# Kernel tuning notes

Measured on AMD Instinct MI355X. Metric: run time of the kernel, lower is better.

Reference implementation:

```python
import jax, jax.numpy as jnp
import numpy as np

J = 3
J_H = 5
C_IN = 128
C_OUT = 128
N0, N1, N2 = 1024, 3072, 2048
DENSITY = 0.01
W_SCALE = 0.02  # keeps P^(2^(J_h-1)) @ x @ W magnitudes reasonable in fp32


def _sym_sparse(key, n, density):
    kv, km = jax.random.split(key)
    mask = jax.random.uniform(km, (n, n)) < density
    a = jnp.where(mask, jax.random.normal(kv, (n, n)), 0.0)
    return jnp.triu(a) + jnp.triu(a, 1).T  # symmetric sparse 'Laplacian'


def _sparse(kv, km, shape, density):
    mask = jax.random.uniform(km, shape) < density
    return jnp.where(mask, jax.random.normal(kv, shape), 0.0)


def setup_inputs() -> dict:
    key = jax.random.key(0)
    ks = jax.random.split(key, 24)
    z0 = jax.random.normal(ks[0], (N0, C_IN), jnp.float32)
    z1 = jax.random.normal(ks[1], (N1, C_IN), jnp.float32)
    z2 = jax.random.normal(ks[2], (N2, C_IN), jnp.float32)
    L0 = _sym_sparse(ks[3], N0, 0.02)
    L1_d = _sym_sparse(ks[4], N1, DENSITY)
    L1_u = _sym_sparse(ks[5], N1, DENSITY)
    L2 = _sym_sparse(ks[6], N2, DENSITY)
    B1 = _sparse(ks[7], ks[8], (N0, N1), DENSITY)
    B2 = _sparse(ks[9], ks[10], (N1, N2), DENSITY)
    W_d = jax.random.normal(ks[11], (J, C_IN, C_OUT)) * W_SCALE
    W_u = jax.random.normal(ks[12], (J, C_IN, C_OUT)) * W_SCALE
    W_h = jax.random.normal(ks[13], (C_IN, C_OUT)) * W_SCALE
    W_b1 = jax.random.normal(ks[14], (J, C_IN, C_OUT)) * W_SCALE
    W_b2 = jax.random.normal(ks[15], (J, C_IN, C_OUT)) * W_SCALE
    attn_d_w = jax.random.normal(ks[16], (1, 2 * C_IN)) * W_SCALE
    attn_d_b = jax.random.normal(ks[17], (1,)) * W_SCALE
    attn_u_w = jax.random.normal(ks[18], (1, 2 * C_IN)) * W_SCALE
    attn_u_b = jax.random.normal(ks[19], (1,)) * W_SCALE
    return dict(z0=z0, z1=z1, z2=z2, L0=L0, L1_d=L1_d, L1_u=L1_u, L2=L2,
                B1=B1, B2=B2, W_d=W_d, W_u=W_u, W_h=W_h, W_b1=W_b1, W_b2=W_b2,
                attn_d_w=attn_d_w, attn_d_b=attn_d_b,
                attn_u_w=attn_u_w, attn_u_b=attn_u_b)


def _attention(x, n, w, b, src, dst):
    # gather edge endpoints -> tiny MLP -> sigmoid -> symmetric scatter
    a = jnp.concatenate([x[src], x[dst]], axis=-1)      # [E, 2C]
    s = jax.nn.sigmoid(a @ w.T + b)[:, 0]               # [E]
    return jnp.zeros((n, n), x.dtype).at[src, dst].set(s).at[dst, src].set(s)


def _harmonic(L, x, W_h):
    lmax = jnp.linalg.eigvalsh(L)[-1]
    # torch does lambda_max.item() -> constant w.r.t. grads
    eps = jax.lax.stop_gradient(jnp.where(lmax > 0, 1.0 / lmax, 0.1))
    P = jnp.eye(L.shape[0], dtype=x.dtype) - eps * L
    for _ in range(J_H - 1):
        P = P @ P                                        # P^(2^(J_h-1))
    return P @ x @ W_h


def reference(z0, z1, z2, L0, L1_d, L1_u, L2, B1, B2,
              W_d, W_u, W_h, W_b1, W_b2,
              attn_d_w, attn_d_b, attn_u_w, attn_u_b):
    # nonzero patterns of the Laplacians (constants, computed on host)
    src_d, dst_d = np.nonzero(np.asarray(jax.device_get(L1_d)))
    src_u, dst_u = np.nonzero(np.asarray(jax.device_get(L1_u)))
    L1d_attn = _attention(z1, N1, attn_d_w, attn_d_b,
                          jnp.asarray(src_d), jnp.asarray(dst_d))
    L1u_attn = _attention(z1, N1, attn_u_w, attn_u_b,
                          jnp.asarray(src_u), jnp.asarray(dst_u))
    # sum_j (A @ z) @ W[j] == (A @ z) @ W.sum(0)
    Wd_s, Wu_s = W_d.sum(0), W_u.sum(0)
    Wb1_s, Wb2_s = W_b1.sum(0), W_b2.sum(0)

    z0_out = (L0 @ z0) @ Wd_s + (B1 @ z1) @ Wb1_s + _harmonic(L0, z0, W_h)
    z0_out = jax.nn.relu(z0_out)

    z1_out = ((L1d_attn @ z1) @ Wd_s + (L1u_attn @ z1) @ Wu_s
              + (B1.T @ z0) @ Wb1_s + (B2 @ z2) @ Wb2_s
              + _harmonic(L1_d + L1_u, z1, W_h))
    z1_out = jax.nn.relu(z1_out)

    z2_out = (L2 @ z2) @ Wu_s + (B2.T @ z1) @ Wb2_s + _harmonic(L2, z2, W_h)
    z2_out = jax.nn.relu(z2_out)
    return (z0_out, z1_out, z2_out)
```

## Files before the change

kernel.cpp:

```cpp
#include <hip/hip_runtime.h>
#include <string.h>

constexpr int M_LZ = 48;

constexpr int CAP_L0 = 26240, CAP_L1 = 118016, CAP_L2 = 52480, CAP_B1 = 39360, CAP_B2 = 78720;
constexpr int CB_L0 = 0;
constexpr int CB_L1D = CB_L0 + CAP_L0;
constexpr int CB_L1U = CB_L1D + CAP_L1;
constexpr int CB_L2  = CB_L1U + CAP_L1;
constexpr int CB_B1  = CB_L2 + CAP_L2;
constexpr int CB_B2  = CB_B1 + CAP_B1;
constexpr int CAP_TOT= CB_B2 + CAP_B2;
constexpr int CB_B1T = CAP_TOT;
constexpr int CB_B2T = CB_B1T + CAP_B1;
constexpr int CAP_TOT2 = CB_B2T + CAP_B2;

constexpr int P_L0=0, P_L1D=1025, P_L1U=4098, P_L2=7171, P_B1=9220, P_B2=10245;
constexpr int P_B1T=13320, P_B2T=16393;
constexpr int C_L0=0, C_L1D=1024, C_L1U=4096, C_L2=7168, C_B1=9216, C_B2=10240;
constexpr int C_B1T=13312, C_B2T=16384;

constexpr size_t HBUF  = (size_t)6144*128;

constexpr size_t W_CNT = 0;
constexpr size_t W_PTR = 18432;
constexpr size_t W_CUR = W_PTR + 18444;
constexpr size_t W_CIDX= W_CUR + 5120;
constexpr size_t W_VAL = W_CIDX + CAP_TOT2;
constexpr size_t W_V0  = W_VAL + CAP_TOT2;
constexpr size_t W_PK  = W_V0 + 6144;
constexpr size_t W_TT  = W_PK + (size_t)64*6144*4;
constexpr size_t W_EPS = W_TT + 6144;
constexpr size_t W_UV  = W_EPS + 128;
constexpr size_t W_H   = W_UV + 4*3072;
constexpr size_t W_SCAT= W_H + 15*HBUF;
constexpr size_t S0_OFF= 0;
constexpr size_t S1_OFF= (size_t)1024*384;
constexpr size_t S2_OFF= S1_OFF + (size_t)3072*640;
constexpr size_t SCAT_TOT = S2_OFF + (size_t)2048*384;
constexpr size_t W_WCAT= W_SCAT + SCAT_TOT;
constexpr size_t WC0=0, WC1=(size_t)384*128, WC2=WC1+(size_t)640*128;
constexpr size_t W_SLOT= W_WCAT + (size_t)1408*128;
constexpr size_t W_FLG = W_SLOT + 1048576;
constexpr size_t W_REL = W_FLG + 65536;

__device__ __forceinline__ float wredf(float v){
  #pragma unroll
  for(int o=32;o;o>>=1) v += __shfl_xor(v,o,64);
  return v;
}
__device__ __forceinline__ int wredi(int v){
  #pragma unroll
  for(int o=32;o;o>>=1) v += __shfl_xor(v,o,64);
  return v;
}
__device__ __forceinline__ void red4x2(float4& a0, float4& a1){
  #pragma unroll
  for (int o=16;o<=32;o<<=1){
    a0.x+=__shfl_xor(a0.x,o,64); a0.y+=__shfl_xor(a0.y,o,64);
    a0.z+=__shfl_xor(a0.z,o,64); a0.w+=__shfl_xor(a0.w,o,64);
    a1.x+=__shfl_xor(a1.x,o,64); a1.y+=__shfl_xor(a1.y,o,64);
    a1.z+=__shfl_xor(a1.z,o,64); a1.w+=__shfl_xor(a1.w,o,64);
  }
}
__device__ __forceinline__ float v0hash(int i, float invs){
  unsigned uu=(unsigned)i*2654435761u; uu^=uu>>16; uu*=2246822519u; uu^=uu>>13;
  return (uu&1)?invs:-invs;
}

__device__ __forceinline__ float ldc(const float* p){
  return __hip_atomic_load(p, __ATOMIC_RELAXED, __HIP_MEMORY_SCOPE_AGENT);
}
__device__ __forceinline__ float2 ldc2(const float* p){
  unsigned long long u = __hip_atomic_load((const unsigned long long*)p,
                          __ATOMIC_RELAXED, __HIP_MEMORY_SCOPE_AGENT);
  float2 r; memcpy(&r,&u,8); return r;
}
__device__ __forceinline__ void stc(float* p, float v){
  __hip_atomic_store(p, v, __ATOMIC_RELAXED, __HIP_MEMORY_SCOPE_AGENT);
}
__device__ __forceinline__ void stc2(float* p, float2 v){
  unsigned long long u; memcpy(&u,&v,8);
  __hip_atomic_store((unsigned long long*)p, u, __ATOMIC_RELAXED, __HIP_MEMORY_SCOPE_AGENT);
}
__device__ __forceinline__ int ldci(const int* p){
  return __hip_atomic_load(p, __ATOMIC_RELAXED, __HIP_MEMORY_SCOPE_AGENT);
}
__device__ __forceinline__ void stci(int* p, int v){
  __hip_atomic_store(p, v, __ATOMIC_RELAXED, __HIP_MEMORY_SCOPE_AGENT);
}

__device__ __forceinline__ void barg(float* ws, int* leafs, int b, int lbase, int Ng,
                                     bool chk, int lidx, int ph){
  const int t = threadIdx.x;
  int* flg = (int*)ws + W_FLG;
  __builtin_amdgcn_s_waitcnt(0);
  __syncthreads();
  if (t==0) stci(flg + (size_t)b*32, ph+1);
  if (chk){
    for (int s=t; s<Ng; s+=256){
      const int* f = flg + (size_t)(lbase+s)*32;
      while (ldci(f) < ph+1) __builtin_amdgcn_s_sleep(1);
    }
    __syncthreads();
    if (t==0){
      #pragma unroll
      for (int i=0;i<16;i++) stci(leafs + (size_t)i*32, ph+1);
    }
    __syncthreads();
  } else {
    if (t==0){
      const int* rl = leafs + (size_t)(lidx&15)*32;
      while (ldci(rl) < ph+1) __builtin_amdgcn_s_sleep(1);
    }
    __syncthreads();
  }
}

__device__ __forceinline__ void bar_lz(float* ws, int b, int grp, int lbase, int Lg,
                                       bool chk, int lb, int ph, int j,
                                       float* shr, float* redm,
                                       float& a_o, float& g_o, float& ib_o){
  const int t = threadIdx.x, lane = t&63, wvv = t>>6;
  __builtin_amdgcn_s_waitcnt(0);
  __syncthreads();
  if (t==0){
    float A0=redm[0]+redm[1]+redm[2]+redm[3];
    float G0=redm[4]+redm[5]+redm[6]+redm[7];
    float N0=redm[8]+redm[9]+redm[10]+redm[11];
    float* sl = ws + W_SLOT + ((size_t)j*2048 + b)*8;
    stc2(sl+2, make_float2(A0,G0)); stc(sl+4, N0);
    __builtin_amdgcn_s_waitcnt(0);
    stci((int*)sl, ph+1);
  }
  if (chk){
    float pa=0.f, pg=0.f, pn=0.f;
    for (int s=t; s<Lg; s+=256){
      const float* sl = ws + W_SLOT + ((size_t)j*2048 + lbase+s)*8;
      while (ldci((const int*)sl) < ph+1) __builtin_amdgcn_s_sleep(1);
      float2 ag = ldc2(sl+2); float nn = ldc(sl+4);
      pa+=ag.x; pg+=ag.y; pn+=nn;
    }
    pa=wredf(pa); pg=wredf(pg); pn=wredf(pn);
    if (lane==0){ shr[0*4+wvv]=pa; shr[1*4+wvv]=pg; shr[2*4+wvv]=pn; }
    __syncthreads();
    if (t==0){
      float a=shr[0]+shr[1]+shr[2]+shr[3];
      float g=shr[4]+shr[5]+shr[6]+shr[7];
      float n=shr[8]+shr[9]+shr[10]+shr[11];
      float ib = 1.f/sqrtf(fmaxf(n - a*a - g*g, 1e-20f));
      float* TT = ws + W_TT + (size_t)(grp*64 + j)*32;
      stc2(TT, make_float2(a,g)); stc(TT+2, n);
      #pragma unroll
      for (int i=0;i<16;i++){
        float* lf = ws + W_REL + (size_t)(grp*16+i)*32;
        stc2(lf+2, make_float2(a,g)); stc(lf+4, ib);
      }
      __builtin_amdgcn_s_waitcnt(0);
      #pragma unroll
      for (int i=0;i<16;i++)
        stci((int*)(ws + W_REL) + (size_t)(grp*16+i)*32, ph+1);
      shr[0]=a; shr[1]=g; shr[2]=ib;
    }
    __syncthreads();
  } else {
    if (t==0){
      const float* lf = ws + W_REL + (size_t)(grp*16 + (lb&15))*32;
      while (ldci((const int*)lf) < ph+1) __builtin_amdgcn_s_sleep(1);
      float2 ag = ldc2(lf+2); float ib = ldc(lf+4);
      shr[0]=ag.x; shr[1]=ag.y; shr[2]=ib;
    }
    __syncthreads();
  }
  a_o = shr[0]; g_o = shr[1]; ib_o = shr[2];
}

__global__ void k_wprep(const float* Wd,const float* Wu,const float* Wh,
                        const float* Wb1,const float* Wb2, float* ws){
  int t = blockIdx.x*256 + threadIdx.x;
  if (t >= 16384) return;
  int* wsi = (int*)ws;
  if (t < 5120) stci(wsi + W_CNT + 13312 + t, 0);
  if (t < 5120) stci(wsi + W_CUR + t, 0);
  for (int i=t; i<65536+2048; i+=16384) wsi[W_FLG+i] = 0;
  for (int i=t; i<131072; i+=16384) wsi[W_SLOT + (size_t)i*8] = 0;
  float sd = Wd[t]  + Wd[16384+t]  + Wd[32768+t];
  float su = Wu[t]  + Wu[16384+t]  + Wu[32768+t];
  float s1 = Wb1[t] + Wb1[16384+t] + Wb1[32768+t];
  float s2 = Wb2[t] + Wb2[16384+t] + Wb2[32768+t];
  float wh = Wh[t];
  float* W0 = ws + W_WCAT + WC0;
  float* W1 = ws + W_WCAT + WC1;
  float* W2 = ws + W_WCAT + WC2;
  W0[t]=sd; W0[16384+t]=s1; W0[32768+t]=wh;
  W1[t]=sd; W1[16384+t]=su; W1[32768+t]=s1; W1[49152+t]=s2; W1[65536+t]=wh;
  W2[t]=su; W2[16384+t]=s2; W2[32768+t]=wh;
}

__device__ __forceinline__ void mat_meta(int wid, const float* L0,const float* L1d,const float* L1u,
    const float* L2,const float* B1,const float* B2,
    const float*& M,int& ncol,int& lrow,int& co,int& po,int& cb,int& cap,int& tco){
  if (wid < 1024){ M=L0;  ncol=1024; lrow=wid;        co=C_L0;  po=P_L0;  cb=CB_L0;  cap=CAP_L0; tco=-1; }
  else if (wid < 4096){ M=L1d; ncol=3072; lrow=wid-1024;  co=C_L1D; po=P_L1D; cb=CB_L1D; cap=CAP_L1; tco=-1; }
  else if (wid < 7168){ M=L1u; ncol=3072; lrow=wid-4096;  co=C_L1U; po=P_L1U; cb=CB_L1U; cap=CAP_L1; tco=-1; }
  else if (wid < 9216){ M=L2;  ncol=2048; lrow=wid-7168;  co=C_L2;  po=P_L2;  cb=CB_L2;  cap=CAP_L2; tco=-1; }
  else if (wid < 10240){ M=B1; ncol=3072; lrow=wid-9216;  co=C_B1;  po=P_B1;  cb=CB_B1;  cap=CAP_B1; tco=C_B1T; }
  else { M=B2; ncol=2048; lrow=wid-10240; co=C_B2;  po=P_B2;  cb=CB_B2;  cap=CAP_B2; tco=C_B2T; }
}

__global__ __launch_bounds__(256,8) void k_all(float* ws,
    const float* z0,const float* z1,const float* z2,
    const float* L0,const float* L1d,const float* L1u,
    const float* L2,const float* B1,const float* B2,
    const float* adw,const float* adb,const float* auw,const float* aub,
    float* out){
  const int b = blockIdx.x, t = threadIdx.x;
  const int wv = t>>6, lane = t&63;
  const int sg = lane>>4, chn = lane&15;
  int* wsi=(int*)ws;
  int* ptrm=wsi+W_PTR; int* cnm=wsi+W_CNT;
  int* cidxm=wsi+W_CIDX; float* valm=ws+W_VAL;

  __shared__ float smem[2616];
  float* Sl  = smem;
  float* Wl  = smem + 544;
  float* TTa = smem;
  float* TTb = smem + 64;
  float* redm= smem + 2592;
  float* shr = smem + 2604;

  int* grel = (int*)ws + W_REL + 48*32;
  int* krel = (int*)ws + W_SLOT + 63*2048*8;

  for (int wid = b*4+wv; wid < 13312; wid += 8192){
    const float* M; int ncol,lrow,co,po,cb,cap,tco;
    mat_meta(wid,L0,L1d,L1u,L2,B1,B2,M,ncol,lrow,co,po,cb,cap,tco);
    const float4* row4 = (const float4*)(M + (size_t)lrow*ncol);
    int c = 0;
    for (int j0=0; j0<ncol; j0+=256){
      float4 v = row4[(j0>>2)+lane];
      int n0=v.x!=0.f, n1=v.y!=0.f, n2=v.z!=0.f, n3=v.w!=0.f;
      c += n0+n1+n2+n3;
      if (tco>=0){
        int jb = j0 + lane*4;
        if (n0) atomicAdd(cnm+tco+jb,   1);
        if (n1) atomicAdd(cnm+tco+jb+1, 1);
        if (n2) atomicAdd(cnm+tco+jb+2, 1);
        if (n3) atomicAdd(cnm+tco+jb+3, 1);
      }
    }
    c = wredi(c);
    if (lane==0) stci(cnm+co+lrow, c);
  }
  barg(ws, grel, b, 0, 2048, b==0, b, 0);

  if (b < 8){
    int* lds = (int*)smem;
    const int rows[8]={1024,3072,3072,2048,1024,3072,3072,2048};
    const int cofs[8]={C_L0,C_L1D,C_L1U,C_L2,C_B1,C_B2,C_B1T,C_B2T};
    const int pofs[8]={P_L0,P_L1D,P_L1U,P_L2,P_B1,P_B2,P_B1T,P_B2T};
    int R=rows[b]; const int* c=cnm+cofs[b]; int* p=ptrm+pofs[b];
    int* cc = (b==6)? (wsi+W_CUR) : (b==7)? (wsi+W_CUR+3072) : nullptr;
    int chunk=(R+255)/256;
    int lo=t*chunk, hi=min(R,lo+chunk);
    int s=0;
    for(int i=lo;i<hi;i++) s+=ldci(c+i);
    lds[t]=(float)0, ((int*)lds)[t]=s; __syncthreads();
    if(t==0){ int run=0; for(int i=0;i<256;i++){int x=((int*)lds)[i];((int*)lds)[i]=run;run+=x;} ((int*)lds)[256]=run; }
    __syncthreads();
    int run=((int*)lds)[t];
    for(int i=lo;i<hi;i++){ stci(p+i, run); if(cc) stci(cc+i, run); run+=ldci(c+i); }
    if(t==0) stci(p+R, ((int*)lds)[256]);
  }
  barg(ws, grel, b, 0, 2048, b==0, b, 1);

  for (int wid = b*4+wv; wid < 13312; wid += 8192){
    const float* M; int ncol,lrow,co,po,cb,cap,tco;
    mat_meta(wid,L0,L1d,L1u,L2,B1,B2,M,ncol,lrow,co,po,cb,cap,tco);
    const float4* row4 = (const float4*)(M + (size_t)lrow*ncol);
    int base = ldci(ptrm+po+lrow);
    int run = 0;
    for (int j0=0; j0<ncol; j0+=256){
      float4 v = row4[(j0>>2)+lane];
      int n0=v.x!=0.f, n1=v.y!=0.f, n2=v.z!=0.f, n3=v.w!=0.f;
      int local = n0+n1+n2+n3;
      int incl = local;
      #pragma unroll
      for (int o=1;o<64;o<<=1){
        int tmp = __shfl_up(incl,o,64);
        if (lane>=o) incl += tmp;
      }
      int tot = __shfl(incl,63,64);
      int pos = base + run + incl - local;
      int jb = j0 + lane*4;
      if (n0){ if(pos<cap){stci(cidxm+cb+pos,jb);   stc(valm+cb+pos,v.x);} pos++; }
      if (n1){ if(pos<cap){stci(cidxm+cb+pos,jb+1); stc(valm+cb+pos,v.y);} pos++; }
      if (n2){ if(pos<cap){stci(cidxm+cb+pos,jb+2); stc(valm+cb+pos,v.z);} pos++; }
      if (n3){ if(pos<cap){stci(cidxm+cb+pos,jb+3); stc(valm+cb+pos,v.w);} pos++; }
      run += tot;
    }
  }
  barg(ws, grel, b, 0, 2048, b==0, b, 2);

  const int* ptr=ptrm; const int* cidx=cidxm; const float* val=valm;

  if (b < 768){
    int g, gbase, nb;
    if (b<128){ g=0; gbase=0;   nb=0;    }
    else if (b<512){ g=1; gbase=128; nb=1024; }
    else { g=2; gbase=512; nb=4096; }
    const int lb = b - gbase;
    const int Lg = (g==0)?128:(g==1)?384:256;
    const bool chk = (lb==0);
    const float invsg = (g==0)?0.03125f:(g==1)?0.0180421959f:0.0220970869f;
    const int hw = lane>>5, hl = lane&31;
    const int p  = lb*8 + wv*2 + hw;
    const int gp = nb + p;
    float a=0.f, gmm=0.f, ib=1.f;
    float vp_m1=0.f, vp_m2=0.f, wp_m1=0.f;
    for (int j=0;j<M_LZ;j++){
      float wp=0.f;
      if (j==0){
        #define GZ(PP,CBB) { const int* rp=ptr+PP; int e=rp[p+1]; \
          for (int k=rp[p]+hl;k<e;k+=32){ wp += val[CBB+k]*v0hash(nb+cidx[CBB+k], invsg); } }
        if (g==0){ GZ(P_L0,CB_L0) }
        else if (g==1){ GZ(P_L1D,CB_L1D) GZ(P_L1U,CB_L1U) }
        else { GZ(P_L2,CB_L2) }
        #undef GZ
      } else {
        const float4* pk = (const float4*)(ws + W_PK) + (size_t)(j-1)*6144 + nb;
        #define GP(PP,CBB) { const int* rp=ptr+PP; int e=rp[p+1]; \
          for (int k=rp[p]+hl;k<e;k+=32){ float v=val[CBB+k]; float4 pq=pk[cidx[CBB+k]]; \
            wp += v*((pq.x - a*pq.y - gmm*pq.z)*ib); } }
        if (g==0){ GP(P_L0,CB_L0) }
        else if (g==1){ GP(P_L1D,CB_L1D) GP(P_L1U,CB_L1U) }
        else { GP(P_L2,CB_L2) }
        #undef GP
      }
      #pragma unroll
      for (int o=16;o;o>>=1) wp += __shfl_xor(wp,o,64);
      float rA=0.f, rG=0.f, rN=0.f;
      if (hl==0){
        float vp;
        if (j==0) vp = v0hash(gp, invsg);
        else      vp = (wp_m1 - a*vp_m1 - gmm*vp_m2)*ib;
        float* pkw = ws + W_PK + ((size_t)j*6144 + gp)*4;
        stc2(pkw, make_float2(wp, vp)); stc(pkw+2, vp_m1);
        rA = vp*wp; rG = vp_m1*wp; rN = wp*wp;
        vp_m2 = vp_m1; vp_m1 = vp; wp_m1 = wp;
      }
      rA += __shfl_xor(rA,32,64); rG += __shfl_xor(rG,32,64); rN += __shfl_xor(rN,32,64);
      if (lane==0){ redm[0*4+wv]=rA; redm[1*4+wv]=rG; redm[2*4+wv]=rN; }
      bar_lz(ws, b, g, gbase, Lg, chk, lb, 1+j, j, shr, redm, a, gmm, ib);
    }
    if (chk && t<64){
      int i = t;
      double lo=1e300, hi=-1e300;
      if (i<M_LZ){
        const float* TT = ws + W_TT + (size_t)(g*64 + i)*32;
        float aa=ldc(TT), gg=ldc(TT+1), nn=ldc(TT+2);
        TTa[i]=aa; TTb[i]=sqrtf(fmaxf(nn-aa*aa-gg*gg,1e-20f));
      }
      if (i<M_LZ){
        double r=(i? fabs((double)TTb[i-1]):0.0) + (i<M_LZ-1? fabs((double)TTb[i]):0.0);
        lo=(double)TTa[i]-r; hi=(double)TTa[i]+r;
      }
      #pragma unroll
      for(int o=32;o;o>>=1){ lo=fmin(lo,__shfl_xor(lo,o,64)); hi=fmax(hi,__shfl_xor(hi,o,64)); }
      lo -= 1.0; hi += 1.0;
      for (int round=0; round<4; round++){
        double x = lo + (hi-lo)*(double)(i+1)/65.0;
        double d = 1.0; int cnt2=0;
        for (int k2=0;k2<M_LZ;k2++){
          double bi = k2? (double)TTb[k2-1] : 0.0;
          d = ((double)TTa[k2]-x) - bi*bi/d;
          if (d==0.0) d = -1e-300;
          if (d<0.0) cnt2++;
        }
        double nlo = (cnt2< M_LZ)? x : -1e300;
        double nhi = (cnt2==M_LZ)? x :  1e300;
        #pragma unroll
        for(int o=32;o;o>>=1){ nlo=fmax(nlo,__shfl_xor(nlo,o,64)); nhi=fmin(nhi,__shfl_xor(nhi,o,64)); }
        if (nlo>-1e299) lo=nlo;
        if (nhi< 1e299) hi=nhi;
      }
      double lam = 0.5*(lo+hi);
      if (i==0) stc(ws+W_EPS+(size_t)g*32, (lam>0.0)? (float)(1.0/lam) : 0.1f);
    }
  } else {
    { int widT = (b-768)*4+wv;
      if (widT < 4096){
        int* cur=wsi+W_CUR;
        if (widT < 1024){
          int r=widT;
          int s0=ldci(ptr+P_B1+r); int e=ldci(ptr+P_B1+r+1);
          for(int k=s0+lane;k<e;k+=64){
            int c=ldci(cidx+CB_B1+k); float v=ldc(val+CB_B1+k);
            int pos=atomicAdd(cur+c,1);
            stci(cidxm+CB_B1T+pos,r); stc(valm+CB_B1T+pos,v);
          }
        } else {
          int r=widT-1024;
          int s0=ldci(ptr+P_B2+r); int e=ldci(ptr+P_B2+r+1);
          for(int k=s0+lane;k<e;k+=64){
            int c=ldci(cidx+CB_B2+k); float v=ldc(val+CB_B2+k);
            int pos=atomicAdd(cur+3072+c,1);
            stci(cidxm+CB_B2T+pos,r); stc(valm+CB_B2T+pos,v);
          }
        }
      }
    }
    const int kb = b - 768;
    const int vw = kb*4 + wv;
    if (vw < 3072){
      float2 x  = ((const float2*)(z1+(size_t)vw*128))[lane];
      float2 a0 = ((const float2*)adw)[lane];
      float2 a1 = ((const float2*)adw)[64+lane];
      float2 b0 = ((const float2*)auw)[lane];
      float2 b1 = ((const float2*)auw)[64+lane];
      float ud=x.x*a0.x+x.y*a0.y, vd=x.x*a1.x+x.y*a1.y;
      float uu=x.x*b0.x+x.y*b0.y, vu=x.x*b1.x+x.y*b1.y;
      ud=wredf(ud); vd=wredf(vd); uu=wredf(uu); vu=wredf(vu);
      if(lane==0){ stc(ws+W_UV+vw,ud); stc(ws+W_UV+3072+vw,vd);
                   stc(ws+W_UV+6144+vw,uu); stc(ws+W_UV+9216+vw,vu); }
    }
    int cgP, nbP, lrP; float e0P;
    if (vw < 3072){ cgP=1; nbP=1024; lrP=vw;      e0P=(1.f/28.f); }
    else          { cgP=2; nbP=4096; lrP=vw-3072; e0P=0.0625f;    }
    const bool has2 = (vw >= 4096);
    const int lr2 = vw - 4096;
    for (int k2=1; k2<=16; k2++){
      const float* ybase = ws + W_H + (size_t)(k2>=2? k2-2:0)*HBUF;
      #define KG2(PP,CBB,NBV,ZZV,LRV) { const int* rp=ptr+PP; int e=rp[(LRV)+1]; \
        for (int kk=rp[LRV]+sg; kk<e; kk+=4){ \
          float v=val[CBB+kk]; int q=cidx[CBB+kk]; \
          const float* sr = (k2==1)? (ZZV)+(size_t)q*128 : ybase+(size_t)((NBV)+q)*128; \
          float4 x0=((const float4*)sr)[chn*2], x1=((const float4*)sr)[chn*2+1]; \
          a0.x+=v*x0.x; a0.y+=v*x0.y; a0.z+=v*x0.z; a0.w+=v*x0.w; \
          a1.x+=v*x1.x; a1.y+=v*x1.y; a1.z+=v*x1.z; a1.w+=v*x1.w; \
        } }
      #define KWRITE(CGV,LRV,GRV,E0V) if (lane<16){ \
          float* dst; \
          if (k2<16) dst = ws + W_H + (size_t)(k2-1)*HBUF + (size_t)(GRV)*128; \
          else { \
            if ((CGV)==0)      dst = ws+W_SCAT+S0_OFF+256 + (size_t)(LRV)*384; \
            else if ((CGV)==1) dst = ws+W_SCAT+S1_OFF+512 + (size_t)(LRV)*640; \
            else               dst = ws+W_SCAT+S2_OFF+256 + (size_t)(LRV)*384; \
          } \
          stc2(dst+chn*8,   make_float2((E0V)*a0.x, (E0V)*a0.y)); \
          stc2(dst+chn*8+2, make_float2((E0V)*a0.z, (E0V)*a0.w)); \
          stc2(dst+chn*8+4, make_float2((E0V)*a1.x, (E0V)*a1.y)); \
          stc2(dst+chn*8+6, make_float2((E0V)*a1.z, (E0V)*a1.w)); }
      {
        float4 a0={0.f,0.f,0.f,0.f}, a1={0.f,0.f,0.f,0.f};
        if (cgP==1){ KG2(P_L1D,CB_L1D,1024,z1,lrP) KG2(P_L1U,CB_L1U,1024,z1,lrP) }
        else { KG2(P_L2,CB_L2,4096,z2,lrP) }
        red4x2(a0,a1);
        KWRITE(cgP, lrP, nbP+lrP, e0P)
      }
      if (has2){
        float4 a0={0.f,0.f,0.f,0.f}, a1={0.f,0.f,0.f,0.f};
        KG2(P_L0,CB_L0,0,z0,lr2)
        red4x2(a0,a1);
        KWRITE(0, lr2, lr2, 0.0625f)
      }
      #undef KG2
      #undef KWRITE
      if (k2<16) barg(ws, krel, b, 768, 1280, b==768, kb, k2+3);
    }
    for (int wid2 = kb*4+wv; wid2 < 18432; wid2 += 5120){
      int task,p2;
      if(wid2<1024){task=0;p2=wid2;}
      else if(wid2<2048){task=1;p2=wid2-1024;}
      else if(wid2<5120){task=2;p2=wid2-2048;}
      else if(wid2<8192){task=3;p2=wid2-5120;}
      else if(wid2<11264){task=4;p2=wid2-8192;}
      else if(wid2<13312){task=5;p2=wid2-11264;}
      else if(wid2<16384){task=6;p2=wid2-13312;}
      else {task=7;p2=wid2-16384;}
      const float* in; const int* rp; int cb2; float* outp; int ostride;
      int mode=0; float Vp=0.f, bb=0.f; const float* U=nullptr;
      switch(task){
        case 0: rp=ptr+P_L0;  cb2=CB_L0;  in=z0; outp=ws+W_SCAT+S0_OFF+0;   ostride=384; break;
        case 1: rp=ptr+P_B1;  cb2=CB_B1;  in=z1; outp=ws+W_SCAT+S0_OFF+128; ostride=384; break;
        case 2: rp=ptr+P_L1D; cb2=CB_L1D; in=z1; outp=ws+W_SCAT+S1_OFF+0;   ostride=640;
                mode=1; U=ws+W_UV; Vp=ldc(ws+W_UV+3072+p2); bb=adb[0]; break;
        case 3: rp=ptr+P_L1U; cb2=CB_L1U; in=z1; outp=ws+W_SCAT+S1_OFF+128; ostride=640;
                mode=1; U=ws+W_UV+6144; Vp=ldc(ws+W_UV+9216+p2); bb=aub[0]; break;
        case 4: rp=ptr+P_B2;  cb2=CB_B2;  in=z2; outp=ws+W_SCAT+S1_OFF+384; ostride=640; break;
        case 5: rp=ptr+P_L2;  cb2=CB_L2;  in=z2; outp=ws+W_SCAT+S2_OFF+0;   ostride=384; break;
        case 6: rp=ptr+P_B1T; cb2=CB_B1T; in=z0; outp=ws+W_SCAT+S1_OFF+256; ostride=640; break;
        default:rp=ptr+P_B2T; cb2=CB_B2T; in=z1; outp=ws+W_SCAT+S2_OFF+128; ostride=384; break;
      }
      float4 a0={0.f,0.f,0.f,0.f}, a1={0.f,0.f,0.f,0.f};
      int e=rp[p2+1];
      for (int k=rp[p2]+sg; k<e; k+=4){
        int q = cidx[cb2+k];
        float v;
        if (mode) v = 1.0f/(1.0f+__expf(-(ldc(U+q)+Vp+bb)));
        else v = val[cb2+k];
        const float* sr = in + (size_t)q*128;
        float4 x0 = ((const float4*)sr)[chn*2];
        float4 x1 = ((const float4*)sr)[chn*2+1];
        a0.x+=v*x0.x; a0.y+=v*x0.y; a0.z+=v*x0.z; a0.w+=v*x0.w;
        a1.x+=v*x1.x; a1.y+=v*x1.y; a1.z+=v*x1.z; a1.w+=v*x1.w;
      }
      red4x2(a0, a1);
      if (sg==0){
        float* dst = outp + (size_t)p2*ostride;
        stc2(dst+chn*8,   make_float2(a0.x,a0.y));
        stc2(dst+chn*8+2, make_float2(a0.z,a0.w));
        stc2(dst+chn*8+4, make_float2(a1.x,a1.y));
        stc2(dst+chn*8+6, make_float2(a1.z,a1.w));
      }
    }
  }

  barg(ws, grel, b, 0, 2048, b==1, b, 30);

  { int r = b*4+wv;
    if (r < 6144){
      int cg = (r<1024)?0:(r<4096)?1:2;
      int lr = r - ((cg==0)?0:(cg==1)?1024:4096);
      const float* zz = (cg==0)?z0:(cg==1)?z1:z2;
      float lam0 = (cg==1)?28.f:16.f;
      float eps  = ldc(ws+W_EPS+(size_t)cg*32);
      float rr = eps*lam0;
      float* hc;
      if (cg==0)      hc = ws+W_SCAT+S0_OFF+256 + (size_t)lr*384;
      else if (cg==1) hc = ws+W_SCAT+S1_OFF+512 + (size_t)lr*640;
      else            hc = ws+W_SCAT+S2_OFF+256 + (size_t)lr*384;
      const float BIN[17] = {1.f,16.f,120.f,560.f,1820.f,4368.f,8008.f,11440.f,12870.f,
                             11440.f,8008.f,4368.f,1820.f,560.f,120.f,16.f,1.f};
      float2 acc = ((const float2*)(zz + (size_t)lr*128))[lane];
      float rk = 1.f;
      #pragma unroll
      for (int k2=1;k2<=15;k2++){
        rk *= -rr;
        float2 y = ((const float2*)(ws + W_H + (size_t)(k2-1)*HBUF + (size_t)r*128))[lane];
        float c = BIN[k2]*rk;
        acc.x += c*y.x; acc.y += c*y.y;
      }
      rk *= -rr;
      float2 y16 = ((const float2*)hc)[lane];
      acc.x += rk*y16.x; acc.y += rk*y16.y;
      stc2(hc + (size_t)lane*2, acc);
    }
  }
  barg(ws, grel, b, 0, 2048, b==1, b, 31);

  if (b < 192){
    const float* S; const float* W; float* outp; int K; int blk;
    if (b<32){       S=ws+W_SCAT+S0_OFF; W=ws+W_WCAT+WC0; outp=out;        K=384; blk=b; }
    else if (b<128){ S=ws+W_SCAT+S1_OFF; W=ws+W_WCAT+WC1; outp=out+131072; K=640; blk=b-32; }
    else {           S=ws+W_SCAT+S2_OFF; W=ws+W_WCAT+WC2; outp=out+524288; K=384; blk=b-128; }
    int r0=blk*32;
    int ty=t>>5, tx=t&31;
    float acc[4][4]={};
    for (int k0=0; k0<K; k0+=16){
      {
        int r=t>>3, kq=(t&7)*2;
        const float* src=S+(size_t)(r0+r)*K + k0+kq;
        Sl[r*17+kq]=src[0]; Sl[r*17+kq+1]=src[1];
      }
      {
        int kk=t>>4, cq=(t&15)*8;
        const float* src=W+(size_t)(k0+kk)*128+cq;
        #pragma unroll
        for(int i=0;i<8;i++) Wl[kk*128+cq+i]=src[i];
      }
      __syncthreads();
      #pragma unroll
      for(int k=0;k<16;k++){
        float sv[4], wvv2[4];
        #pragma unroll
        for(int i=0;i<4;i++) sv[i]=Sl[(ty*4+i)*17+k];
        #pragma unroll
        for(int i=0;i<4;i++) wvv2[i]=Wl[k*128+tx+32*i];
        #pragma unroll
        for(int a2=0;a2<4;a2++)
          #pragma unroll
          for(int b2=0;b2<4;b2++) acc[a2][b2]+=sv[a2]*wvv2[b2];
      }
      __syncthreads();
    }
    #pragma unroll
    for(int a2=0;a2<4;a2++)
      #pragma unroll
      for(int b2=0;b2<4;b2++){
        int r=r0+ty*4+a2, col=tx+32*b2;
        outp[(size_t)r*128+col]=fmaxf(acc[a2][b2],0.f);
      }
  }
}

extern "C" void kernel_launch(void* const* d_in, const int* in_sizes, int n_in,
                              void* d_out, int out_size, void* d_ws, size_t ws_size,
                              hipStream_t stream){
  const float* z0 =(const float*)d_in[0];
  const float* z1 =(const float*)d_in[1];
  const float* z2 =(const float*)d_in[2];
  const float* L0 =(const float*)d_in[3];
  const float* L1d=(const float*)d_in[4];
  const float* L1u=(const float*)d_in[5];
  const float* L2 =(const float*)d_in[6];
  const float* B1 =(const float*)d_in[7];
  const float* B2 =(const float*)d_in[8];
  const float* Wd =(const float*)d_in[9];
  const float* Wu =(const float*)d_in[10];
  const float* Wh =(const float*)d_in[11];
  const float* Wb1=(const float*)d_in[12];
  const float* Wb2=(const float*)d_in[13];
  const float* adw=(const float*)d_in[14];
  const float* adb=(const float*)d_in[15];
  const float* auw=(const float*)d_in[16];
  const float* aub=(const float*)d_in[17];
  float* ws=(float*)d_ws;
  float* out=(float*)d_out;

  hipLaunchKernelGGL(k_wprep, dim3(64), dim3(256), 0, stream, Wd,Wu,Wh,Wb1,Wb2,ws);
  hipLaunchKernelGGL(k_all, dim3(2048), dim3(256), 0, stream,
                     ws, z0, z1, z2, L0, L1d, L1u, L2, B1, B2,
                     adw, adb, auw, aub, out);
}
```

Baseline: 804.3 us.

## Defer B1/B2 CSR build to non-Lanczos blocks to overlap with eigen estimation

The dense-to-CSR count, prefix and fill for the incidence matrices B1 and B2 (plus their transposes) leave the initial grid-wide phases and move into the block group that runs in parallel with the Lanczos blocks, after its Chebyshev/power iterations. The early global barriers then cover only the Laplacians, so the Lanczos eigenvalue estimation can start sooner. The cost is four extra group barriers in the second block group and longer work on that side, which could become the new critical path. Helper functions are factored out for count, fill and prefix.

```diff
diff --git a/kernel.cpp b/kernel.cpp
--- a/kernel.cpp
+++ b/kernel.cpp
@@ -208,6 +208,70 @@
   else { M=B2; ncol=2048; lrow=wid-10240; co=C_B2;  po=P_B2;  cb=CB_B2;  cap=CAP_B2; tco=C_B2T; }
 }
 
+__device__ __forceinline__ void do_count(int wid, const float* L0,const float* L1d,const float* L1u,
+    const float* L2,const float* B1,const float* B2, int* cnm, int lane){
+  const float* M; int ncol,lrow,co,po,cb,cap,tco;
+  mat_meta(wid,L0,L1d,L1u,L2,B1,B2,M,ncol,lrow,co,po,cb,cap,tco);
+  const float4* row4 = (const float4*)(M + (size_t)lrow*ncol);
+  int c = 0;
+  for (int j0=0; j0<ncol; j0+=256){
+    float4 v = row4[(j0>>2)+lane];
+    int n0=v.x!=0.f, n1=v.y!=0.f, n2=v.z!=0.f, n3=v.w!=0.f;
+    c += n0+n1+n2+n3;
+    if (tco>=0){
+      int jb = j0 + lane*4;
+      if (n0) atomicAdd(cnm+tco+jb,   1);
+      if (n1) atomicAdd(cnm+tco+jb+1, 1);
+      if (n2) atomicAdd(cnm+tco+jb+2, 1);
+      if (n3) atomicAdd(cnm+tco+jb+3, 1);
+    }
+  }
+  c = wredi(c);
+  if (lane==0) stci(cnm+co+lrow, c);
+}
+
+__device__ __forceinline__ void do_fill(int wid, const float* L0,const float* L1d,const float* L1u,
+    const float* L2,const float* B1,const float* B2,
+    int* ptrm, int* cidxm, float* valm, int lane){
+  const float* M; int ncol,lrow,co,po,cb,cap,tco;
+  mat_meta(wid,L0,L1d,L1u,L2,B1,B2,M,ncol,lrow,co,po,cb,cap,tco);
+  const float4* row4 = (const float4*)(M + (size_t)lrow*ncol);
+  int base = ldci(ptrm+po+lrow);
+  int run = 0;
+  for (int j0=0; j0<ncol; j0+=256){
+    float4 v = row4[(j0>>2)+lane];
+    int n0=v.x!=0.f, n1=v.y!=0.f, n2=v.z!=0.f, n3=v.w!=0.f;
+    int local = n0+n1+n2+n3;
+    int incl = local;
+    #pragma unroll
+    for (int o=1;o<64;o<<=1){
+      int tmp = __shfl_up(incl,o,64);
+      if (lane>=o) incl += tmp;
+    }
+    int tot = __shfl(incl,63,64);
+    int pos = base + run + incl - local;
+    int jb = j0 + lane*4;
+    if (n0){ if(pos<cap){stci(cidxm+cb+pos,jb);   stc(valm+cb+pos,v.x);} pos++; }
+    if (n1){ if(pos<cap){stci(cidxm+cb+pos,jb+1); stc(valm+cb+pos,v.y);} pos++; }
+    if (n2){ if(pos<cap){stci(cidxm+cb+pos,jb+2); stc(valm+cb+pos,v.z);} pos++; }
+    if (n3){ if(pos<cap){stci(cidxm+cb+pos,jb+3); stc(valm+cb+pos,v.w);} pos++; }
+    run += tot;
+  }
+}
+
+__device__ __forceinline__ void do_prefix(int R, const int* c, int* p, int* cc, int* lds, int t){
+  int chunk=(R+255)/256;
+  int lo=t*chunk, hi=min(R,lo+chunk);
+  int s=0;
+  for(int i=lo;i<hi;i++) s+=ldci(c+i);
+  lds[t]=s; __syncthreads();
+  if(t==0){ int run=0; for(int i=0;i<256;i++){int x=lds[i];lds[i]=run;run+=x;} lds[256]=run; }
+  __syncthreads();
+  int run=lds[t];
+  for(int i=lo;i<hi;i++){ stci(p+i, run); if(cc) stci(cc+i, run); run+=ldci(c+i); }
+  if(t==0) stci(p+R, lds[256]);
+}
+
 __global__ __launch_bounds__(256,8) void k_all(float* ws,
     const float* z0,const float* z1,const float* z2,
     const float* L0,const float* L1d,const float* L1u,
@@ -232,74 +296,21 @@
   int* grel = (int*)ws + W_REL + 48*32;
   int* krel = (int*)ws + W_SLOT + 63*2048*8;
 
-  for (int wid = b*4+wv; wid < 13312; wid += 8192){
-    const float* M; int ncol,lrow,co,po,cb,cap,tco;
-    mat_meta(wid,L0,L1d,L1u,L2,B1,B2,M,ncol,lrow,co,po,cb,cap,tco);
-    const float4* row4 = (const float4*)(M + (size_t)lrow*ncol);
-    int c = 0;
-    for (int j0=0; j0<ncol; j0+=256){
-      float4 v = row4[(j0>>2)+lane];
-      int n0=v.x!=0.f, n1=v.y!=0.f, n2=v.z!=0.f, n3=v.w!=0.f;
-      c += n0+n1+n2+n3;
-      if (tco>=0){
-        int jb = j0 + lane*4;
-        if (n0) atomicAdd(cnm+tco+jb,   1);
-        if (n1) atomicAdd(cnm+tco+jb+1, 1);
-        if (n2) atomicAdd(cnm+tco+jb+2, 1);
-        if (n3) atomicAdd(cnm+tco+jb+3, 1);
-      }
-    }
-    c = wredi(c);
-    if (lane==0) stci(cnm+co+lrow, c);
-  }
+  for (int wid = b*4+wv; wid < 9216; wid += 8192)
+    do_count(wid, L0,L1d,L1u,L2,B1,B2, cnm, lane);
   barg(ws, grel, b, 0, 2048, b==0, b, 0);
 
-  if (b < 8){
+  if (b < 4){
     int* lds = (int*)smem;
-    const int rows[8]={1024,3072,3072,2048,1024,3072,3072,2048};
-    const int cofs[8]={C_L0,C_L1D,C_L1U,C_L2,C_B1,C_B2,C_B1T,C_B2T};
-    const int pofs[8]={P_L0,P_L1D,P_L1U,P_L2,P_B1,P_B2,P_B1T,P_B2T};
-    int R=rows[b]; const int* c=cnm+cofs[b]; int* p=ptrm+pofs[b];
-    int* cc = (b==6)? (wsi+W_CUR) : (b==7)? (wsi+W_CUR+3072) : nullptr;
-    int chunk=(R+255)/256;
-    int lo=t*chunk, hi=min(R,lo+chunk);
-    int s=0;
-    for(int i=lo;i<hi;i++) s+=ldci(c+i);
-    lds[t]=(float)0, ((int*)lds)[t]=s; __syncthreads();
-    if(t==0){ int run=0; for(int i=0;i<256;i++){int x=((int*)lds)[i];((int*)lds)[i]=run;run+=x;} ((int*)lds)[256]=run; }
-    __syncthreads();
-    int run=((int*)lds)[t];
-    for(int i=lo;i<hi;i++){ stci(p+i, run); if(cc) stci(cc+i, run); run+=ldci(c+i); }
-    if(t==0) stci(p+R, ((int*)lds)[256]);
+    const int rows[4]={1024,3072,3072,2048};
+    const int cofs[4]={C_L0,C_L1D,C_L1U,C_L2};
+    const int pofs[4]={P_L0,P_L1D,P_L1U,P_L2};
+    do_prefix(rows[b], cnm+cofs[b], ptrm+pofs[b], nullptr, lds, t);
   }
   barg(ws, grel, b, 0, 2048, b==0, b, 1);
 
-  for (int wid = b*4+wv; wid < 13312; wid += 8192){
-    const float* M; int ncol,lrow,co,po,cb,cap,tco;
-    mat_meta(wid,L0,L1d,L1u,L2,B1,B2,M,ncol,lrow,co,po,cb,cap,tco);
-    const float4* row4 = (const float4*)(M + (size_t)lrow*ncol);
-    int base = ldci(ptrm+po+lrow);
-    int run = 0;
-    for (int j0=0; j0<ncol; j0+=256){
-      float4 v = row4[(j0>>2)+lane];
-      int n0=v.x!=0.f, n1=v.y!=0.f, n2=v.z!=0.f, n3=v.w!=0.f;
-      int local = n0+n1+n2+n3;
-      int incl = local;
-      #pragma unroll
-      for (int o=1;o<64;o<<=1){
-        int tmp = __shfl_up(incl,o,64);
-        if (lane>=o) incl += tmp;
-      }
-      int tot = __shfl(incl,63,64);
-      int pos = base + run + incl - local;
-      int jb = j0 + lane*4;
-      if (n0){ if(pos<cap){stci(cidxm+cb+pos,jb);   stc(valm+cb+pos,v.x);} pos++; }
-      if (n1){ if(pos<cap){stci(cidxm+cb+pos,jb+1); stc(valm+cb+pos,v.y);} pos++; }
-      if (n2){ if(pos<cap){stci(cidxm+cb+pos,jb+2); stc(valm+cb+pos,v.z);} pos++; }
-      if (n3){ if(pos<cap){stci(cidxm+cb+pos,jb+3); stc(valm+cb+pos,v.w);} pos++; }
-      run += tot;
-    }
-  }
+  for (int wid = b*4+wv; wid < 9216; wid += 8192)
+    do_fill(wid, L0,L1d,L1u,L2,B1,B2, ptrm, cidxm, valm, lane);
   barg(ws, grel, b, 0, 2048, b==0, b, 2);
 
   const int* ptr=ptrm; const int* cidx=cidxm; const float* val=valm;
@@ -388,28 +399,6 @@
       if (i==0) stc(ws+W_EPS+(size_t)g*32, (lam>0.0)? (float)(1.0/lam) : 0.1f);
     }
   } else {
-    { int widT = (b-768)*4+wv;
-      if (widT < 4096){
-        int* cur=wsi+W_CUR;
-        if (widT < 1024){
-          int r=widT;
-          int s0=ldci(ptr+P_B1+r); int e=ldci(ptr+P_B1+r+1);
-          for(int k=s0+lane;k<e;k+=64){
-            int c=ldci(cidx+CB_B1+k); float v=ldc(val+CB_B1+k);
-            int pos=atomicAdd(cur+c,1);
-            stci(cidxm+CB_B1T+pos,r); stc(valm+CB_B1T+pos,v);
-          }
-        } else {
-          int r=widT-1024;
-          int s0=ldci(ptr+P_B2+r); int e=ldci(ptr+P_B2+r+1);
-          for(int k=s0+lane;k<e;k+=64){
-            int c=ldci(cidx+CB_B2+k); float v=ldc(val+CB_B2+k);
-            int pos=atomicAdd(cur+3072+c,1);
-            stci(cidxm+CB_B2T+pos,r); stc(valm+CB_B2T+pos,v);
-          }
-        }
-      }
-    }
     const int kb = b - 768;
     const int vw = kb*4 + wv;
     if (vw < 3072){
@@ -468,6 +457,47 @@
       #undef KWRITE
       if (k2<16) barg(ws, krel, b, 768, 1280, b==768, kb, k2+3);
     }
+    { int widB = 9216 + kb*4 + wv;
+      if (widB < 13312) do_count(widB, L0,L1d,L1u,L2,B1,B2, cnm, lane);
+    }
+    barg(ws, krel, b, 768, 1280, b==768, kb, 19);
+    if (b >= 768 && b < 772){
+      int* lds = (int*)smem;
+      const int rows[4]={1024,3072,3072,2048};
+      const int cofs[4]={C_B1,C_B2,C_B1T,C_B2T};
+      const int pofs[4]={P_B1,P_B2,P_B1T,P_B2T};
+      int bi = b-768;
+      int* cc = (bi==2)? (wsi+W_CUR) : (bi==3)? (wsi+W_CUR+3072) : nullptr;
+      do_prefix(rows[bi], cnm+cofs[bi], ptrm+pofs[bi], cc, lds, t);
+    }
+    barg(ws, krel, b, 768, 1280, b==768, kb, 20);
+    { int widB = 9216 + kb*4 + wv;
+      if (widB < 13312) do_fill(widB, L0,L1d,L1u,L2,B1,B2, ptrm, cidxm, valm, lane);
+    }
+    barg(ws, krel, b, 768, 1280, b==768, kb, 21);
+    { int widT = kb*4+wv;
+      if (widT < 4096){
+        int* cur=wsi+W_CUR;
+        if (widT < 1024){
+          int r=widT;
+          int s0=ldci(ptr+P_B1+r); int e=ldci(ptr+P_B1+r+1);
+          for(int k=s0+lane;k<e;k+=64){
+            int c=ldci(cidx+CB_B1+k); float v=ldc(val+CB_B1+k);
+            int pos=atomicAdd(cur+c,1);
+            stci(cidxm+CB_B1T+pos,r); stc(valm+CB_B1T+pos,v);
+          }
+        } else {
+          int r=widT-1024;
+          int s0=ldci(ptr+P_B2+r); int e=ldci(ptr+P_B2+r+1);
+          for(int k=s0+lane;k<e;k+=64){
+            int c=ldci(cidx+CB_B2+k); float v=ldc(val+CB_B2+k);
+            int pos=atomicAdd(cur+3072+c,1);
+            stci(cidxm+CB_B2T+pos,r); stc(valm+CB_B2T+pos,v);
+          }
+        }
+      }
+    }
+    barg(ws, krel, b, 768, 1280, b==768, kb, 22);
     for (int wid2 = kb*4+wv; wid2 < 18432; wid2 += 5120){
       int task,p2;
       if(wid2<1024){task=0;p2=wid2;}
```

New measurement: 782.3 us. -2.7%, faster.

## Stage compacted row nonzeros in scratch to avoid second dense matrix scan

Applied to the files above, without the earlier changes.

The dense-to-CSR conversion previously read every dense matrix twice: once to count nonzeros per row and once to write column indices and values. Now the first pass also wave-compacts each row's nonzeros into a per-row scratch slot of 128 entries, placed in the harmonic buffer region. After the prefix sum, the second pass only copies those staged entries to their final CSR offsets. This removes the second full read of about 130 MB of dense input. The cost is extra scratch writes, and any row with more than 128 nonzeros would be silently truncated.

```diff
diff --git a/kernel.cpp b/kernel.cpp
--- a/kernel.cpp
+++ b/kernel.cpp
@@ -33,6 +33,8 @@
 constexpr size_t W_EPS = W_TT + 6144;
 constexpr size_t W_UV  = W_EPS + 128;
 constexpr size_t W_H   = W_UV + 4*3072;
+constexpr size_t W_SCI = W_H;
+constexpr size_t W_SCV = W_H + (size_t)13312*128;
 constexpr size_t W_SCAT= W_H + 15*HBUF;
 constexpr size_t S0_OFF= 0;
 constexpr size_t S1_OFF= (size_t)1024*384;
@@ -208,6 +210,72 @@
   else { M=B2; ncol=2048; lrow=wid-10240; co=C_B2;  po=P_B2;  cb=CB_B2;  cap=CAP_B2; tco=C_B2T; }
 }
 
+__device__ __forceinline__ void do_scanA(int wid, const float* L0,const float* L1d,const float* L1u,
+    const float* L2,const float* B1,const float* B2, float* ws, int* cnm, int lane){
+  int* wsi=(int*)ws;
+  const float* M; int ncol,lrow,co,po,cb,cap,tco;
+  mat_meta(wid,L0,L1d,L1u,L2,B1,B2,M,ncol,lrow,co,po,cb,cap,tco);
+  const float4* row4 = (const float4*)(M + (size_t)lrow*ncol);
+  int* sci = wsi + W_SCI + (size_t)wid*128;
+  float* scv = ws + W_SCV + (size_t)wid*128;
+  int run = 0;
+  for (int j0=0; j0<ncol; j0+=256){
+    float4 v = row4[(j0>>2)+lane];
+    int n0=v.x!=0.f, n1=v.y!=0.f, n2=v.z!=0.f, n3=v.w!=0.f;
+    int local = n0+n1+n2+n3;
+    int incl = local;
+    #pragma unroll
+    for (int o=1;o<64;o<<=1){
+      int tmp = __shfl_up(incl,o,64);
+      if (lane>=o) incl += tmp;
+    }
+    int tot = __shfl(incl,63,64);
+    int pos = run + incl - local;
+    int jb = j0 + lane*4;
+    if (n0){ if(pos<128){stci(sci+pos,jb);   stc(scv+pos,v.x);} pos++; }
+    if (n1){ if(pos<128){stci(sci+pos,jb+1); stc(scv+pos,v.y);} pos++; }
+    if (n2){ if(pos<128){stci(sci+pos,jb+2); stc(scv+pos,v.z);} pos++; }
+    if (n3){ if(pos<128){stci(sci+pos,jb+3); stc(scv+pos,v.w);} pos++; }
+    if (tco>=0){
+      if (n0) atomicAdd(cnm+tco+jb,   1);
+      if (n1) atomicAdd(cnm+tco+jb+1, 1);
+      if (n2) atomicAdd(cnm+tco+jb+2, 1);
+      if (n3) atomicAdd(cnm+tco+jb+3, 1);
+    }
+    run += tot;
+  }
+  if (lane==0) stci(cnm+co+lrow, run);
+}
+
+__device__ __forceinline__ void do_writeB(int wid, const float* L0,const float* L1d,const float* L1u,
+    const float* L2,const float* B1,const float* B2,
+    float* ws, int* ptrm, int* cnm, int* cidxm, float* valm, int lane){
+  int* wsi=(int*)ws;
+  const float* M; int ncol,lrow,co,po,cb,cap,tco;
+  mat_meta(wid,L0,L1d,L1u,L2,B1,B2,M,ncol,lrow,co,po,cb,cap,tco);
+  const int* sci = wsi + W_SCI + (size_t)wid*128;
+  const float* scv = ws + W_SCV + (size_t)wid*128;
+  int base = ldci(ptrm+po+lrow);
+  int rn = ldci(cnm+co+lrow); if (rn>128) rn=128;
+  for (int k=lane; k<rn; k+=64){
+    int pos = base+k;
+    if (pos<cap){ stci(cidxm+cb+pos, ldci(sci+k)); stc(valm+cb+pos, ldc(scv+k)); }
+  }
+}
+
+__device__ __forceinline__ void do_prefix(int R, const int* c, int* p, int* cc, int* lds, int t){
+  int chunk=(R+255)/256;
+  int lo=t*chunk, hi=min(R,lo+chunk);
+  int s=0;
+  for(int i=lo;i<hi;i++) s+=ldci(c+i);
+  lds[t]=s; __syncthreads();
+  if(t==0){ int run=0; for(int i=0;i<256;i++){int x=lds[i];lds[i]=run;run+=x;} lds[256]=run; }
+  __syncthreads();
+  int run=lds[t];
+  for(int i=lo;i<hi;i++){ stci(p+i, run); if(cc) stci(cc+i, run); run+=ldci(c+i); }
+  if(t==0) stci(p+R, lds[256]);
+}
+
 __global__ __launch_bounds__(256,8) void k_all(float* ws,
     const float* z0,const float* z1,const float* z2,
     const float* L0,const float* L1d,const float* L1u,
@@ -232,26 +300,8 @@
   int* grel = (int*)ws + W_REL + 48*32;
   int* krel = (int*)ws + W_SLOT + 63*2048*8;
 
-  for (int wid = b*4+wv; wid < 13312; wid += 8192){
-    const float* M; int ncol,lrow,co,po,cb,cap,tco;
-    mat_meta(wid,L0,L1d,L1u,L2,B1,B2,M,ncol,lrow,co,po,cb,cap,tco);
-    const float4* row4 = (const float4*)(M + (size_t)lrow*ncol);
-    int c = 0;
-    for (int j0=0; j0<ncol; j0+=256){
-      float4 v = row4[(j0>>2)+lane];
-      int n0=v.x!=0.f, n1=v.y!=0.f, n2=v.z!=0.f, n3=v.w!=0.f;
-      c += n0+n1+n2+n3;
-      if (tco>=0){
-        int jb = j0 + lane*4;
-        if (n0) atomicAdd(cnm+tco+jb,   1);
-        if (n1) atomicAdd(cnm+tco+jb+1, 1);
-        if (n2) atomicAdd(cnm+tco+jb+2, 1);
-        if (n3) atomicAdd(cnm+tco+jb+3, 1);
-      }
-    }
-    c = wredi(c);
-    if (lane==0) stci(cnm+co+lrow, c);
-  }
+  for (int wid = b*4+wv; wid < 13312; wid += 8192)
+    do_scanA(wid, L0,L1d,L1u,L2,B1,B2, ws, cnm, lane);
   barg(ws, grel, b, 0, 2048, b==0, b, 0);
 
   if (b < 8){
@@ -259,47 +309,13 @@
     const int rows[8]={1024,3072,3072,2048,1024,3072,3072,2048};
     const int cofs[8]={C_L0,C_L1D,C_L1U,C_L2,C_B1,C_B2,C_B1T,C_B2T};
     const int pofs[8]={P_L0,P_L1D,P_L1U,P_L2,P_B1,P_B2,P_B1T,P_B2T};
-    int R=rows[b]; const int* c=cnm+cofs[b]; int* p=ptrm+pofs[b];
     int* cc = (b==6)? (wsi+W_CUR) : (b==7)? (wsi+W_CUR+3072) : nullptr;
-    int chunk=(R+255)/256;
-    int lo=t*chunk, hi=min(R,lo+chunk);
-    int s=0;
-    for(int i=lo;i<hi;i++) s+=ldci(c+i);
-    lds[t]=(float)0, ((int*)lds)[t]=s; __syncthreads();
-    if(t==0){ int run=0; for(int i=0;i<256;i++){int x=((int*)lds)[i];((int*)lds)[i]=run;run+=x;} ((int*)lds)[256]=run; }
-    __syncthreads();
-    int run=((int*)lds)[t];
-    for(int i=lo;i<hi;i++){ stci(p+i, run); if(cc) stci(cc+i, run); run+=ldci(c+i); }
-    if(t==0) stci(p+R, ((int*)lds)[256]);
+    do_prefix(rows[b], cnm+cofs[b], ptrm+pofs[b], cc, lds, t);
   }
   barg(ws, grel, b, 0, 2048, b==0, b, 1);
 
-  for (int wid = b*4+wv; wid < 13312; wid += 8192){
-    const float* M; int ncol,lrow,co,po,cb,cap,tco;
-    mat_meta(wid,L0,L1d,L1u,L2,B1,B2,M,ncol,lrow,co,po,cb,cap,tco);
-    const float4* row4 = (const float4*)(M + (size_t)lrow*ncol);
-    int base = ldci(ptrm+po+lrow);
-    int run = 0;
-    for (int j0=0; j0<ncol; j0+=256){
-      float4 v = row4[(j0>>2)+lane];
-      int n0=v.x!=0.f, n1=v.y!=0.f, n2=v.z!=0.f, n3=v.w!=0.f;
-      int local = n0+n1+n2+n3;
-      int incl = local;
-      #pragma unroll
-      for (int o=1;o<64;o<<=1){
-        int tmp = __shfl_up(incl,o,64);
-        if (lane>=o) incl += tmp;
-      }
-      int tot = __shfl(incl,63,64);
-      int pos = base + run + incl - local;
-      int jb = j0 + lane*4;
-      if (n0){ if(pos<cap){stci(cidxm+cb+pos,jb);   stc(valm+cb+pos,v.x);} pos++; }
-      if (n1){ if(pos<cap){stci(cidxm+cb+pos,jb+1); stc(valm+cb+pos,v.y);} pos++; }
-      if (n2){ if(pos<cap){stci(cidxm+cb+pos,jb+2); stc(valm+cb+pos,v.z);} pos++; }
-      if (n3){ if(pos<cap){stci(cidxm+cb+pos,jb+3); stc(valm+cb+pos,v.w);} pos++; }
-      run += tot;
-    }
-  }
+  for (int wid = b*4+wv; wid < 13312; wid += 8192)
+    do_writeB(wid, L0,L1d,L1u,L2,B1,B2, ws, ptrm, cnm, cidxm, valm, lane);
   barg(ws, grel, b, 0, 2048, b==0, b, 2);
 
   const int* ptr=ptrm; const int* cidx=cidxm; const float* val=valm;
```

Result: faster. 762.5 us (-5.2%).
